# Optimization experiments

Measured on AMD Instinct MI355X. Metric: run time of the kernel, lower is better.

The kernel has to match this reference:

```python
import jax, jax.numpy as jnp
import numpy as np

HIDDEN = 2048
N_HEADS = 16
N_KV = 4
HEAD_DIM = 128
B, T = 2, 2048


def setup_inputs() -> dict:
    key = jax.random.key(0)
    k1, k2, k3, k4 = jax.random.split(key, 4)
    x = jax.random.normal(k1, (B, T, HIDDEN), dtype=jnp.float32)
    # linear weights stored [out, in] like torch; we apply x @ W.T
    w_q = jax.random.normal(k2, (N_HEADS * HEAD_DIM, HIDDEN), dtype=jnp.float32) * (HIDDEN ** -0.5)
    w_kv = jax.random.normal(k3, (2 * N_KV * HEAD_DIM, HIDDEN), dtype=jnp.float32) * (HIDDEN ** -0.5)
    w_o = jax.random.normal(k4, (HIDDEN, N_HEADS * HEAD_DIM), dtype=jnp.float32) * ((N_HEADS * HEAD_DIM) ** -0.5)
    return {"x": x, "w_q": w_q, "w_kv": w_kv, "w_o": w_o}


def reference(x, w_q, w_kv, w_o):
    b, t, _ = x.shape
    groups = N_HEADS // N_KV
    scale = HEAD_DIM ** -0.5

    q = (x @ w_q.T).reshape(b, t, N_HEADS, HEAD_DIM).transpose(0, 2, 1, 3)  # [B,H,T,D]
    kv = x @ w_kv.T
    k, v = jnp.split(kv, 2, axis=-1)
    k = k.reshape(b, t, N_KV, HEAD_DIM).transpose(0, 2, 1, 3)  # [B,KV,T,D]
    v = v.reshape(b, t, N_KV, HEAD_DIM).transpose(0, 2, 1, 3)
    # repeat_interleave over head dim -> [B,H,T,D]
    k = jnp.repeat(k, groups, axis=1)
    v = jnp.repeat(v, groups, axis=1)

    scores = jnp.einsum('bhqd,bhkd->bhqk', q, k) * scale  # [B,H,T,T]
    causal = jnp.triu(jnp.ones((t, t), dtype=bool), k=1)
    scores = jnp.where(causal, -jnp.inf, scores)
    weights = jax.nn.softmax(scores, axis=-1)
    out = jnp.einsum('bhqk,bhkd->bhqd', weights, v)  # [B,H,T,D]
    out = out.transpose(0, 2, 1, 3).reshape(b, t, N_HEADS * HEAD_DIM)
    return out @ w_o.T
```

## Files before the change

kernel.cpp:

```cpp
#include <hip/hip_runtime.h>

typedef short bf16x8 __attribute__((ext_vector_type(8)));
typedef float f32x4 __attribute__((ext_vector_type(4)));

__device__ __forceinline__ unsigned short f2bf(float f) {
    unsigned int u = __float_as_uint(f);
    u = (u + 0x7fff + ((u >> 16) & 1)) >> 16;
    return (unsigned short)u;
}
__device__ __forceinline__ float bf2f(short s) {
    return __uint_as_float(((unsigned int)(unsigned short)s) << 16);
}

__device__ __forceinline__ void async16(const void* g, void* l) {
    __builtin_amdgcn_global_load_lds(
        (const __attribute__((address_space(1))) void*)g,
        (__attribute__((address_space(3))) void*)l,
        16 , 0 , 0 );
}

__global__ void castk(const float* __restrict__ in, unsigned short* __restrict__ out, int n4) {
    int i = blockIdx.x * blockDim.x + threadIdx.x;
    if (i < n4) {
        float4 f = ((const float4*)in)[i];
        ushort4 u;
        u.x = f2bf(f.x); u.y = f2bf(f.y); u.z = f2bf(f.z); u.w = f2bf(f.w);
        ((ushort4*)out)[i] = u;
    }
}

template <typename OutT>
__global__ __launch_bounds__(256) void gemm_bt(const unsigned short* __restrict__ A,
                                               const unsigned short* __restrict__ B,
                                               OutT* __restrict__ C,
                                               int M, int N, int K,
                                               int ncut, float qscale) {
    __shared__ unsigned short As[128 * 32];
    __shared__ unsigned short Bs[128 * 32];
    const int tid  = threadIdx.x;
    const int lane = tid & 63;
    const int w    = tid >> 6;
    const int quad = lane >> 4;
    const int l16  = lane & 15;
    const int wr   = w >> 1;
    const int wc   = w & 1;
    const int m0 = blockIdx.x * 128;
    const int n0 = blockIdx.y * 128;

    f32x4 acc[4][4] = {};

    const int srow = 16 * w + (lane >> 2);
    const int scol = (lane & 3) * 8;
    const unsigned short* Ag = A + (size_t)(m0 + srow) * K + scol;
    const unsigned short* Bg = B + (size_t)(n0 + srow) * K + scol;
    unsigned short* AsW = &As[(16 * w) * 32];
    unsigned short* BsW = &Bs[(16 * w) * 32];

    for (int k0 = 0; k0 < K; k0 += 32) {
        async16(Ag + k0,                  AsW);
        async16(Ag + (size_t)64 * K + k0, AsW + 64 * 32);
        async16(Bg + k0,                  BsW);
        async16(Bg + (size_t)64 * K + k0, BsW + 64 * 32);
        __syncthreads();

        bf16x8 af[4], bfr[4];
#pragma unroll
        for (int mt = 0; mt < 4; ++mt)
            af[mt] = *(const bf16x8*)&As[(wr * 64 + mt * 16 + l16) * 32 + quad * 8];
#pragma unroll
        for (int nt = 0; nt < 4; ++nt)
            bfr[nt] = *(const bf16x8*)&Bs[(wc * 64 + nt * 16 + l16) * 32 + quad * 8];
#pragma unroll
        for (int mt = 0; mt < 4; ++mt)
#pragma unroll
            for (int nt = 0; nt < 4; ++nt)
                acc[mt][nt] = __builtin_amdgcn_mfma_f32_16x16x32_bf16(af[mt], bfr[nt], acc[mt][nt], 0, 0, 0);
        __syncthreads();
    }

#pragma unroll
    for (int mt = 0; mt < 4; ++mt) {
        int row = m0 + wr * 64 + mt * 16 + quad * 4;
#pragma unroll
        for (int nt = 0; nt < 4; ++nt) {
            int col = n0 + wc * 64 + nt * 16 + l16;
            f32x4 v = acc[mt][nt];
            float s = (col < ncut) ? qscale : 1.0f;
#pragma unroll
            for (int j = 0; j < 4; ++j) {
                float vj = v[j] * s;
                if constexpr (sizeof(OutT) == 4)
                    C[(size_t)(row + j) * N + col] = vj;
                else
                    C[(size_t)(row + j) * N + col] = f2bf(vj);
            }
        }
    }
}

__global__ __launch_bounds__(256) void transpose_v(const unsigned short* __restrict__ QKV,
                                                   unsigned short* __restrict__ Vt) {
    __shared__ unsigned short Ls[64 * 136];
    const int tid = threadIdx.x;
    const int k0  = blockIdx.x * 64;
    const int b   = blockIdx.y >> 2;
    const int kvh = blockIdx.y & 3;

#pragma unroll
    for (int pass = 0; pass < 4; ++pass) {
        int c = tid + pass * 256;
        int key = c >> 4, dc = (c & 15) * 8;
        bf16x8 v = *(const bf16x8*)(QKV + (size_t)(b * 2048 + k0 + key) * 3072 + 2560 + kvh * 128 + dc);
        *(bf16x8*)&Ls[key * 136 + dc] = v;
    }
    __syncthreads();
#pragma unroll
    for (int pass = 0; pass < 4; ++pass) {
        int c = tid + pass * 256;
        int d = c >> 3, kc = (c & 7) * 8;
        bf16x8 v;
#pragma unroll
        for (int i = 0; i < 8; ++i) v[i] = (short)Ls[(kc + i) * 136 + d];
        *(bf16x8*)(Vt + ((size_t)(b * 4 + kvh) * 128 + d) * 2048 + k0 + kc) = v;
    }
}

__global__ __launch_bounds__(256, 2) void attn_fwd5(const unsigned short* __restrict__ QKV,
                                                    const unsigned short* __restrict__ Vt,
                                                    unsigned short* __restrict__ Opart,
                                                    float* __restrict__ lpart) {
    __shared__ __attribute__((aligned(16))) unsigned short Ks[2][64 * 128];
    __shared__ __attribute__((aligned(16))) unsigned short Vs[2][128 * 64];
    __shared__ __attribute__((aligned(16))) unsigned short Ps[4][32 * 64];

    const int tid  = threadIdx.x;
    const int lane = tid & 63;
    const int w    = tid >> 6;
    const int quad = lane >> 4;
    const int l16  = lane & 15;
    const int swz  = (l16 & 7) << 3;

    const int hb   = blockIdx.x;
    const int h    = hb & 15;
    const int b    = hb >> 4;
    const int y    = blockIdx.y;
    const int p    = 15 - (y >> 1);
    const int half = y & 1;
    const int kvh  = h >> 2;
    const float M_FIX = 12.0f;

    const int ntot   = p + 1;
    const int tstart = half ? ntot : 0;
    const int tend   = half ? 2 * ntot : ntot;

    const int qbase = p * 128;
    const int qw0   = qbase + w * 32;
    const int qw1   = qw0 + 16;

    bf16x8 qf[2][4];
#pragma unroll
    for (int g = 0; g < 2; ++g)
#pragma unroll
        for (int kd = 0; kd < 4; ++kd)
            qf[g][kd] = *(const bf16x8*)(QKV + (size_t)(b * 2048 + qw0 + g * 16 + l16) * 3072
                                         + h * 128 + kd * 32 + quad * 8);

    f32x4 oacc[2][8] = {};
    float rs[2][4] = {};

    const unsigned short* gk[4];
    const unsigned short* gv[4];
#pragma unroll
    for (int pp = 0; pp < 4; ++pp) {
        int r  = (4 * w + pp) * 4 + (lane >> 4);
        int s  = lane & 15;
        int sp = (s & 8) | ((s ^ r) & 7);
        gk[pp] = QKV + (size_t)(b * 2048 + r) * 3072 + 2048 + kvh * 128 + sp * 8;
        int d  = (4 * w + pp) * 8 + (lane >> 3);
        int sv = (lane & 7) ^ (d & 7);
        gv[pp] = Vt + ((size_t)(b * 4 + kvh) * 128 + d) * 2048 + sv * 8;
    }

    unsigned short* Pw = &Ps[w][0];

    auto stage = [&](int nb, int t) {
        const size_t ko = (size_t)t * 64;
#pragma unroll
        for (int pp = 0; pp < 4; ++pp) {
            async16(gk[pp] + ko * 3072, &Ks[nb][(4 * w + pp) * 512]);
            async16(gv[pp] + ko,        &Vs[nb][(4 * w + pp) * 512]);
        }
    };

    stage(0, tstart);
    int cur = 0;

    for (int t = tstart; t < tend; ++t) {
        __syncthreads();
        if (t + 1 < tend) stage(cur ^ 1, t + 1);
        const int k0 = t * 64;

        if (k0 <= qw0 + 15) {
            const bool live1 = (k0 <= qw1 + 15);

            f32x4 sacc[2][4] = {};
            __builtin_amdgcn_s_setprio(1);
#pragma unroll
            for (int kt = 0; kt < 4; ++kt) {
                bf16x8 kf[4];
#pragma unroll
                for (int kd = 0; kd < 4; ++kd)
                    kf[kd] = *(const bf16x8*)&Ks[cur][(kt * 16 + l16) * 128
                                                      + ((kd * 32 + quad * 8) ^ swz)];
#pragma unroll
                for (int kd = 0; kd < 4; ++kd)
                    sacc[0][kt] = __builtin_amdgcn_mfma_f32_16x16x32_bf16(qf[0][kd], kf[kd], sacc[0][kt], 0, 0, 0);
                if (live1) {
#pragma unroll
                    for (int kd = 0; kd < 4; ++kd)
                        sacc[1][kt] = __builtin_amdgcn_mfma_f32_16x16x32_bf16(qf[1][kd], kf[kd], sacc[1][kt], 0, 0, 0);
                }
            }
            __builtin_amdgcn_s_setprio(0);

#pragma unroll
            for (int g = 0; g < 2; ++g) {
                if (g == 1 && !live1) continue;
                const int qwg = qw0 + g * 16;
                const bool diag = (k0 + 63 > qwg);
#pragma unroll
                for (int j = 0; j < 4; ++j) {
                    int qrow = qwg + quad * 4 + j;
                    int prow = g * 16 + quad * 4 + j;
                    int psw  = (prow & 7) << 3;
#pragma unroll
                    for (int kt = 0; kt < 4; ++kt) {
                        float pv = __expf(sacc[g][kt][j] - M_FIX);
                        if (diag) {
                            int key = k0 + kt * 16 + l16;
                            if (key > qrow) pv = 0.f;
                        }
                        rs[g][j] += pv;
                        Pw[prow * 64 + ((kt * 16 + l16) ^ psw)] = f2bf(pv);
                    }
                }
            }

            bf16x8 pf[2][2];
#pragma unroll
            for (int g = 0; g < 2; ++g) {
                if (g == 1 && !live1) continue;
#pragma unroll
                for (int ks = 0; ks < 2; ++ks)
                    pf[g][ks] = *(const bf16x8*)&Pw[(g * 16 + l16) * 64
                                                    + ((ks * 32 + quad * 8) ^ swz)];
            }
            __builtin_amdgcn_s_setprio(1);
#pragma unroll
            for (int dt = 0; dt < 8; ++dt) {
                bf16x8 vf[2];
#pragma unroll
                for (int ks = 0; ks < 2; ++ks)
                    vf[ks] = *(const bf16x8*)&Vs[cur][(dt * 16 + l16) * 64
                                                      + ((ks * 32 + quad * 8) ^ swz)];
#pragma unroll
                for (int ks = 0; ks < 2; ++ks)
                    oacc[0][dt] = __builtin_amdgcn_mfma_f32_16x16x32_bf16(pf[0][ks], vf[ks], oacc[0][dt], 0, 0, 0);
                if (live1) {
#pragma unroll
                    for (int ks = 0; ks < 2; ++ks)
                        oacc[1][dt] = __builtin_amdgcn_mfma_f32_16x16x32_bf16(pf[1][ks], vf[ks], oacc[1][dt], 0, 0, 0);
                }
            }
            __builtin_amdgcn_s_setprio(0);
        }
        cur ^= 1;
    }

#pragma unroll
    for (int g = 0; g < 2; ++g) {
#pragma unroll
        for (int j = 0; j < 4; ++j) {
            float r = rs[g][j];
#pragma unroll
            for (int off = 1; off < 16; off <<= 1)
                r += __shfl_xor(r, off, 64);
            if (l16 == 0)
                lpart[((size_t)(half * 2 + b) * 16 + h) * 2048 + qw0 + g * 16 + quad * 4 + j] = r;
        }
#pragma unroll
        for (int dt = 0; dt < 8; ++dt)
#pragma unroll
            for (int j = 0; j < 4; ++j) {
                int qrow = qw0 + g * 16 + quad * 4 + j;
                Opart[(size_t)(half * 4096 + b * 2048 + qrow) * 2048 + h * 128 + dt * 16 + l16] =
                    f2bf(oacc[g][dt][j]);
            }
    }
}

__global__ __launch_bounds__(256) void combine(const unsigned short* __restrict__ Opart,
                                               const float* __restrict__ lpart,
                                               unsigned short* __restrict__ O) {
    const int r   = blockIdx.x;
    const int b   = r >> 11, row = r & 2047;
    const int col = threadIdx.x * 8;
    const int h   = col >> 7;
    bf16x8 a = *(const bf16x8*)(Opart + (size_t)r * 2048 + col);
    bf16x8 c = *(const bf16x8*)(Opart + (size_t)(4096 + r) * 2048 + col);
    float la = lpart[((size_t)(0 * 2 + b) * 16 + h) * 2048 + row];
    float lb = lpart[((size_t)(1 * 2 + b) * 16 + h) * 2048 + row];
    float inv = 1.0f / (la + lb);
    bf16x8 o;
#pragma unroll
    for (int i = 0; i < 8; ++i)
        o[i] = (short)f2bf((bf2f(a[i]) + bf2f(c[i])) * inv);
    *(bf16x8*)(O + (size_t)r * 2048 + col) = o;
}

extern "C" void kernel_launch(void* const* d_in, const int* in_sizes, int n_in,
                              void* d_out, int out_size, void* d_ws, size_t ws_size,
                              hipStream_t stream) {
    const float* x   = (const float*)d_in[0];
    const float* wq  = (const float*)d_in[1];
    const float* wkv = (const float*)d_in[2];
    const float* wo  = (const float*)d_in[3];
    float* out = (float*)d_out;

    char* ws = (char*)d_ws;
    size_t off = 0;
    auto alloc = [&](size_t bytes) { size_t o = off; off += (bytes + 255) & ~(size_t)255; return o; };
    unsigned short* xb    = (unsigned short*)(ws + alloc((size_t)4096 * 2048 * 2));
    unsigned short* wqkvb = (unsigned short*)(ws + alloc((size_t)3072 * 2048 * 2));
    unsigned short* wob   = (unsigned short*)(ws + alloc((size_t)2048 * 2048 * 2));
    unsigned short* QKVb  = (unsigned short*)(ws + alloc((size_t)4096 * 3072 * 2));
    unsigned short* Ab    = (unsigned short*)(ws + alloc((size_t)4096 * 2048 * 2));
    unsigned short* Vtb   = (unsigned short*)(ws + alloc((size_t)2 * 4 * 128 * 2048 * 2));
    unsigned short* Opart = (unsigned short*)(ws + alloc((size_t)2 * 4096 * 2048 * 2));
    float*          lpart = (float*)(ws + alloc((size_t)2 * 2 * 16 * 2048 * 4));

    const float qscale = 0.08838834764831845f;

    castk<<<8192, 256, 0, stream>>>(x,   xb,    4096 * 2048 / 4);
    castk<<<4096, 256, 0, stream>>>(wq,  wqkvb, 2048 * 2048 / 4);
    castk<<<2048, 256, 0, stream>>>(wkv, wqkvb + (size_t)2048 * 2048, 1024 * 2048 / 4);
    castk<<<4096, 256, 0, stream>>>(wo,  wob,   2048 * 2048 / 4);

    gemm_bt<unsigned short><<<dim3(32, 24), 256, 0, stream>>>(xb, wqkvb, QKVb, 4096, 3072, 2048, 2048, qscale);

    transpose_v<<<dim3(32, 8), 256, 0, stream>>>(QKVb, Vtb);

    attn_fwd5<<<dim3(32, 32), 256, 0, stream>>>(QKVb, Vtb, Opart, lpart);
    combine<<<4096, 256, 0, stream>>>(Opart, lpart, Ab);

    gemm_bt<float><<<dim3(32, 16), 256, 0, stream>>>(Ab, wob, out, 4096, 2048, 2048, 0, 1.0f);
}
```

Before: 311.3 us.

## Replace GEMM with double-buffered 256-row tile kernel using swizzled LDS and prefetch

Replaces the simple 128x128 single-buffered GEMM with a 512-thread kernel that uses 256-row tiles, a K-step of 64 and double-buffered LDS. The next tile is loaded with async global-to-LDS copies, interleaved between MFMA phases under hand-placed waitcnt and barriers. LDS uses an XOR swizzle to avoid bank conflicts, and s_setprio raises priority around the MFMA blocks. The QKV GEMM uses 256x256 tiles and the output GEMM 256x128, which trades fewer blocks (192 and 256 workgroups) for more reuse per block. The manual vmcnt accounting is fragile and could break if the compiler reorders the loads.

```diff
diff --git a/kernel.cpp b/kernel.cpp
--- a/kernel.cpp
+++ b/kernel.cpp
@@ -29,62 +29,115 @@
     }
 }
 
-template <typename OutT>
-__global__ __launch_bounds__(256) void gemm_bt(const unsigned short* __restrict__ A,
-                                               const unsigned short* __restrict__ B,
-                                               OutT* __restrict__ C,
-                                               int M, int N, int K,
-                                               int ncut, float qscale) {
-    __shared__ unsigned short As[128 * 32];
-    __shared__ unsigned short Bs[128 * 32];
+template <int NREP, typename OutT>
+__global__ __launch_bounds__(512, 2) void gemm8p(const unsigned short* __restrict__ A,
+                                                 const unsigned short* __restrict__ B,
+                                                 OutT* __restrict__ C,
+                                                 int N, int K, int NT,
+                                                 int ncut, float qscale) {
+    constexpr int NCH = 4 + NREP;
+    __shared__ __attribute__((aligned(16))) unsigned short LA[2][256 * 64];
+    __shared__ __attribute__((aligned(16))) unsigned short LB[2][NREP * 64 * 64];
+
     const int tid  = threadIdx.x;
     const int lane = tid & 63;
     const int w    = tid >> 6;
     const int quad = lane >> 4;
     const int l16  = lane & 15;
-    const int wr   = w >> 1;
-    const int wc   = w & 1;
-    const int m0 = blockIdx.x * 128;
-    const int n0 = blockIdx.y * 128;
-
-    f32x4 acc[4][4] = {};
-
-    const int srow = 16 * w + (lane >> 2);
-    const int scol = (lane & 3) * 8;
-    const unsigned short* Ag = A + (size_t)(m0 + srow) * K + scol;
-    const unsigned short* Bg = B + (size_t)(n0 + srow) * K + scol;
-    unsigned short* AsW = &As[(16 * w) * 32];
-    unsigned short* BsW = &Bs[(16 * w) * 32];
-
-    for (int k0 = 0; k0 < K; k0 += 32) {
-        async16(Ag + k0,                  AsW);
-        async16(Ag + (size_t)64 * K + k0, AsW + 64 * 32);
-        async16(Bg + k0,                  BsW);
-        async16(Bg + (size_t)64 * K + k0, BsW + 64 * 32);
-        __syncthreads();
-
-        bf16x8 af[4], bfr[4];
-#pragma unroll
-        for (int mt = 0; mt < 4; ++mt)
-            af[mt] = *(const bf16x8*)&As[(wr * 64 + mt * 16 + l16) * 32 + quad * 8];
-#pragma unroll
-        for (int nt = 0; nt < 4; ++nt)
-            bfr[nt] = *(const bf16x8*)&Bs[(wc * 64 + nt * 16 + l16) * 32 + quad * 8];
-#pragma unroll
-        for (int mt = 0; mt < 4; ++mt)
-#pragma unroll
-            for (int nt = 0; nt < 4; ++nt)
-                acc[mt][nt] = __builtin_amdgcn_mfma_f32_16x16x32_bf16(af[mt], bfr[nt], acc[mt][nt], 0, 0, 0);
-        __syncthreads();
-    }
-
-#pragma unroll
-    for (int mt = 0; mt < 4; ++mt) {
-        int row = m0 + wr * 64 + mt * 16 + quad * 4;
-#pragma unroll
-        for (int nt = 0; nt < 4; ++nt) {
-            int col = n0 + wc * 64 + nt * 16 + l16;
-            f32x4 v = acc[mt][nt];
+    const int wm   = w >> 2;
+    const int wn   = w & 3;
+    const int m0   = blockIdx.x * 256;
+    const int n0   = blockIdx.y * (NREP * 64);
+    const int swz  = (l16 & 7) << 3;
+
+    const int lr = lane >> 3;
+    const int ls = lane & 7;
+    const int ss = ls ^ lr;
+    const unsigned short* aSrc = A + (size_t)(m0 + w * 8 + lr) * K + ss * 8;
+    const unsigned short* bSrc = B + (size_t)(n0 + w * 8 + lr) * K + ss * 8;
+
+    f32x4 acc[8][NREP] = {};
+
+    auto stage1 = [&](int nb, int t, int si) {
+        if (si >= NCH) return;
+        if (si < NREP) {
+            async16(bSrc + (size_t)si * 64 * K + t * 64, &LB[nb][(si * 64 + w * 8) * 64]);
+        } else {
+            int j = si - NREP;
+            int c = (j == 0) ? 0 : (j == 1) ? 2 : (j == 2) ? 1 : 3;
+            async16(aSrc + (size_t)c * 64 * K + t * 64, &LA[nb][(c * 64 + w * 8) * 64]);
+        }
+    };
+
+    auto readA = [&](int cur, int q, bf16x8 af[2][2]) {
+#pragma unroll
+        for (int mi = 0; mi < 2; ++mi)
+#pragma unroll
+            for (int kk = 0; kk < 2; ++kk)
+                af[mi][kk] = *(const bf16x8*)&LA[cur][(size_t)(wm * 128 + (q * 2 + mi) * 16 + l16) * 64
+                                                      + ((kk * 32 + quad * 8) ^ swz)];
+    };
+
+    auto domfma = [&](int q, bf16x8 af[2][2], bf16x8 (&bf)[NREP][2]) {
+        __builtin_amdgcn_s_setprio(1);
+#pragma unroll
+        for (int mi = 0; mi < 2; ++mi)
+#pragma unroll
+            for (int n = 0; n < NREP; ++n)
+#pragma unroll
+                for (int kk = 0; kk < 2; ++kk)
+                    acc[q * 2 + mi][n] = __builtin_amdgcn_mfma_f32_16x16x32_bf16(
+                        af[mi][kk], bf[n][kk], acc[q * 2 + mi][n], 0, 0, 0);
+        __builtin_amdgcn_s_setprio(0);
+    };
+
+    auto ktile = [&](int cur, int tn, bool last) {
+        bf16x8 bf[NREP][2];
+        bf16x8 af0[2][2], af1[2][2], af2[2][2], af3[2][2];
+        asm volatile("s_waitcnt vmcnt(2)" ::: "memory");
+        if (!last) { stage1(cur ^ 1, tn, 0); stage1(cur ^ 1, tn, 1); }
+        asm volatile("s_barrier" ::: "memory");
+#pragma unroll
+        for (int n = 0; n < NREP; ++n)
+#pragma unroll
+            for (int kk = 0; kk < 2; ++kk)
+                bf[n][kk] = *(const bf16x8*)&LB[cur][(size_t)(wn * (NREP * 16) + n * 16 + l16) * 64
+                                                     + ((kk * 32 + quad * 8) ^ swz)];
+        readA(cur, 0, af0);
+        domfma(0, af0, bf);
+        readA(cur, 1, af1);
+        if (!last) { stage1(cur ^ 1, tn, 2); stage1(cur ^ 1, tn, 3); }
+        asm volatile("s_barrier" ::: "memory");
+        domfma(1, af1, bf);
+        if (last) asm volatile("s_waitcnt vmcnt(0)" ::: "memory");
+        else      asm volatile("s_waitcnt vmcnt(4)" ::: "memory");
+        if (!last) { stage1(cur ^ 1, tn, 4); stage1(cur ^ 1, tn, 5); }
+        asm volatile("s_barrier" ::: "memory");
+        readA(cur, 2, af2);
+        domfma(2, af2, bf);
+        readA(cur, 3, af3);
+        if (!last) { stage1(cur ^ 1, tn, 6); stage1(cur ^ 1, tn, 7); }
+        asm volatile("s_barrier" ::: "memory");
+        domfma(3, af3, bf);
+    };
+
+#pragma unroll
+    for (int s = 0; s < NCH; ++s) stage1(0, 0, s);
+
+    int cur = 0;
+    for (int t = 0; t < NT - 1; ++t) {
+        ktile(cur, t + 1, false);
+        cur ^= 1;
+    }
+    ktile(cur, 0, true);
+
+#pragma unroll
+    for (int m = 0; m < 8; ++m) {
+        int row = m0 + wm * 128 + m * 16 + quad * 4;
+#pragma unroll
+        for (int n = 0; n < NREP; ++n) {
+            int col = n0 + wn * (NREP * 16) + n * 16 + l16;
+            f32x4 v = acc[m][n];
             float s = (col < ncut) ? qscale : 1.0f;
 #pragma unroll
             for (int j = 0; j < 4; ++j) {
@@ -346,12 +399,12 @@
     castk<<<2048, 256, 0, stream>>>(wkv, wqkvb + (size_t)2048 * 2048, 1024 * 2048 / 4);
     castk<<<4096, 256, 0, stream>>>(wo,  wob,   2048 * 2048 / 4);
 
-    gemm_bt<unsigned short><<<dim3(32, 24), 256, 0, stream>>>(xb, wqkvb, QKVb, 4096, 3072, 2048, 2048, qscale);
+    gemm8p<4, unsigned short><<<dim3(16, 12), 512, 0, stream>>>(xb, wqkvb, QKVb, 3072, 2048, 32, 2048, qscale);
 
     transpose_v<<<dim3(32, 8), 256, 0, stream>>>(QKVb, Vtb);
 
     attn_fwd5<<<dim3(32, 32), 256, 0, stream>>>(QKVb, Vtb, Opart, lpart);
     combine<<<4096, 256, 0, stream>>>(Opart, lpart, Ab);
 
-    gemm_bt<float><<<dim3(32, 16), 256, 0, stream>>>(Ab, wob, out, 4096, 2048, 2048, 0, 1.0f);
-}
+    gemm8p<2, float><<<dim3(16, 16), 512, 0, stream>>>(Ab, wob, out, 2048, 2048, 32, 0, 1.0f);
+}
```

Result: no change. 305.4 us (-1.9%).
